# Kernel tuning notes

Hardware: AMD Instinct MI355X
Metric: run time of the kernel (lower is better)

## Reference

```python
import math
import jax, jax.numpy as jnp
import numpy as np

# dims: batch, in-channels, out-channels, features (freq bins), frames, heads, expansion
B, C, CO, F, W, NH, EXP = 1, 8, 8, 512, 256, 8, 4
CC = C + CO          # channels into cross-attn query (cat of h and self_attn)
FC = C + 2 * CO      # channels into FFN (cat of h, self_attn, src_attn)
FH = F * EXP         # FFN hidden features


def mc_linear(x, pw, dw=None):
    # x: [B,Cin,Fin,W]; pw: [Cin,Fout,Fin] per-channel positionwise matmul;
    # dw: [Cout,Cin] channel-mixing matmul ('depthwise' in the repo's naming)
    y = jnp.einsum('bcfw,cgf->bcgw', x, pw)
    if dw is not None:
        y = jnp.einsum('bcgw,oc->bogw', y, dw)
    return y


def frame_conv(x, w, b):
    # Conv2d kernel (1,3), padding (0,1): 1D conv along the frame axis
    y = jax.lax.conv_general_dilated(x, w, (1, 1), ((0, 0), (1, 1)),
                                     dimension_numbers=('NCHW', 'OIHW', 'NCHW'))
    return y + b[None, :, None, None]


def mc_layernorm(x, g, b, eps=1e-5):
    # normalize over the feature axis (2), per (batch, channel, frame)
    mu = x.mean(axis=2, keepdims=True)
    var = jnp.mean(jnp.square(x - mu), axis=2, keepdims=True)
    return (x - mu) * jax.lax.rsqrt(var + eps) * g[None, :, :, None] + b[None, :, :, None]


def mc_attention(xq, xkv, q_pw, q_dw, q_cw, q_cb, k_pw, k_cw, k_cb, v_pw, v_cw, v_cb, o_pw):
    q = frame_conv(mc_linear(xq, q_pw, q_dw), q_cw, q_cb)   # [B,CO,F,Wq]
    k = frame_conv(mc_linear(xkv, k_pw), k_cw, k_cb)        # [B,CO,F,Wk]
    v = frame_conv(mc_linear(xkv, v_pw), v_cw, v_cb)
    dh = F // NH

    def heads(t):  # [B,CO,F,Wt] -> [B,CO,NH,Wt,dh]
        b_, c_, f_, w_ = t.shape
        return t.transpose(0, 1, 3, 2).reshape(b_, c_, w_, NH, dh).transpose(0, 1, 3, 2, 4)

    qh, kh, vh = heads(q), heads(k), heads(v)
    qk = jnp.einsum('bchqd,bchkd->bchqk', qh, kh) / math.sqrt(F)
    a = jnp.einsum('bchqk,bchkd->bchqd', jax.nn.softmax(qk, axis=-1), vh)
    b_, c_, h_, w_, _ = a.shape
    a = a.transpose(0, 1, 3, 2, 4).reshape(b_, c_, w_, F).transpose(0, 1, 3, 2)  # [B,CO,F,Wq]
    return mc_linear(a, o_pw), qk


def setup_inputs() -> dict:
    key = jax.random.key(0)
    ks = jax.random.split(key, 32)
    it = iter(range(32))

    def rn(shape, s=0.02):
        return jax.random.normal(ks[next(it)], shape, jnp.float32) * s

    inp = {
        'x': jax.random.normal(ks[next(it)], (B, C, F, W), jnp.float32),
        'src': jax.random.normal(ks[next(it)], (B, C, F, W), jnp.float32),
        'ln_g': jnp.ones((C, F), jnp.float32),
        'ln_b': jnp.zeros((C, F), jnp.float32),
        # self-attention (C -> CO, C == CO so no channel-mix on projections)
        'sa_q_pw': rn((C, F, F)), 'sa_q_cw': rn((CO, CO, 1, 3), 0.1), 'sa_q_cb': jnp.zeros((CO,), jnp.float32),
        'sa_k_pw': rn((C, F, F)), 'sa_k_cw': rn((CO, CO, 1, 3), 0.1), 'sa_k_cb': jnp.zeros((CO,), jnp.float32),
        'sa_v_pw': rn((C, F, F)), 'sa_v_cw': rn((CO, CO, 1, 3), 0.1), 'sa_v_cb': jnp.zeros((CO,), jnp.float32),
        'sa_o_pw': rn((CO, F, F)),
        # cross-attention (query from CC=C+CO channels -> CO; key/value from src with C channels)
        'ca_q_pw': rn((CC, F, F)), 'ca_q_dw': rn((CO, CC), 0.1),
        'ca_q_cw': rn((CO, CO, 1, 3), 0.1), 'ca_q_cb': jnp.zeros((CO,), jnp.float32),
        'ca_k_pw': rn((C, F, F)), 'ca_k_cw': rn((CO, CO, 1, 3), 0.1), 'ca_k_cb': jnp.zeros((CO,), jnp.float32),
        'ca_v_pw': rn((C, F, F)), 'ca_v_cw': rn((CO, CO, 1, 3), 0.1), 'ca_v_cb': jnp.zeros((CO,), jnp.float32),
        'ca_o_pw': rn((CO, F, F)),
        # FFN
        'ffn1_pw': rn((FC, FH, F)), 'ffn1_dw': rn((FC, FC), 0.1),
        'ffn2_pw': rn((FC, F, FH)), 'ffn2_dw': rn((C, FC), 0.1),
    }
    return inp


def reference(x, src, ln_g, ln_b,
              sa_q_pw, sa_q_cw, sa_q_cb, sa_k_pw, sa_k_cw, sa_k_cb, sa_v_pw, sa_v_cw, sa_v_cb, sa_o_pw,
              ca_q_pw, ca_q_dw, ca_q_cw, ca_q_cb, ca_k_pw, ca_k_cw, ca_k_cb, ca_v_pw, ca_v_cw, ca_v_cb, ca_o_pw,
              ffn1_pw, ffn1_dw, ffn2_pw, ffn2_dw):
    h = mc_layernorm(x, ln_g, ln_b)
    sa, qk1 = mc_attention(h, h, sa_q_pw, None, sa_q_cw, sa_q_cb,
                           sa_k_pw, sa_k_cw, sa_k_cb, sa_v_pw, sa_v_cw, sa_v_cb, sa_o_pw)
    ca, qk2 = mc_attention(jnp.concatenate([h, sa], axis=1), src,
                           ca_q_pw, ca_q_dw, ca_q_cw, ca_q_cb,
                           ca_k_pw, ca_k_cw, ca_k_cb, ca_v_pw, ca_v_cw, ca_v_cb, ca_o_pw)
    z = mc_linear(jnp.concatenate([h, sa, ca], axis=1), ffn1_pw, ffn1_dw)
    z = jax.nn.gelu(z, approximate=False)
    z = mc_linear(z, ffn2_pw, ffn2_dw)
    return (x + z, qk1, qk2)
```

## Files before the change

### kernel.cpp

```cpp
#include <hip/hip_runtime.h>
#include <math.h>

typedef __attribute__((ext_vector_type(4))) float f32x4;
typedef __attribute__((ext_vector_type(8))) short s16x8;
typedef __attribute__((ext_vector_type(4))) short s16x4;

__device__ __forceinline__ unsigned short f2b(float f) {
    union { float f; unsigned u; } v; v.f = f;
    unsigned r = v.u + 0x7fffu + ((v.u >> 16) & 1u);
    return (unsigned short)(r >> 16);
}
__device__ __forceinline__ float b2f(unsigned short u) {
    union { unsigned u; float f; } v; v.u = ((unsigned)u) << 16;
    return v.f;
}

__device__ __forceinline__ void gll16(const void* g, void* l) {
    __builtin_amdgcn_global_load_lds((const __attribute__((address_space(1))) unsigned int*)g,
                                     (__attribute__((address_space(3))) unsigned int*)l,
                                     16, 0, 0);
}

constexpr int kF = 512;
constexpr int kW = 256;
constexpr int kFW = kF * kW;

__global__ __launch_bounds__(256) void prep_kernel(const float* __restrict__ x,
                                                   const float* __restrict__ g,
                                                   const float* __restrict__ b,
                                                   unsigned short* __restrict__ hTb,
                                                   const float* __restrict__ src,
                                                   unsigned short* __restrict__ SRCT) {
    __shared__ float tile[64][65];
    __shared__ float s1[16][16], s2[16][16];
    int bid = blockIdx.x;
    int t = threadIdx.x;
    if (bid < 128) {
        int c = bid >> 4;
        int w0 = (bid & 15) * 16;
        int wi = t & 15, fg = t >> 4;
        const float* xb = x + (size_t)c * kFW + w0 + wi;
        float sum = 0.f, sum2 = 0.f;
        for (int j = 0; j < 32; ++j) {
            float v = xb[(size_t)(fg * 32 + j) * kW];
            sum += v; sum2 += v * v;
        }
        s1[fg][wi] = sum; s2[fg][wi] = sum2;
        __syncthreads();
        float ts = 0.f, tq = 0.f;
        #pragma unroll
        for (int j = 0; j < 16; ++j) { ts += s1[j][wi]; tq += s2[j][wi]; }
        float mu = ts * (1.0f / 512.0f);
        float rstd = rsqrtf(tq * (1.0f / 512.0f) - mu * mu + 1e-5f);
        const float* gc = g + c * kF + fg * 32;
        const float* bc = b + c * kF + fg * 32;
        unsigned short* ob = hTb + (size_t)c * kFW + (size_t)(w0 + wi) * kF + fg * 32;
        for (int j = 0; j < 32; j += 4) {
            float v0 = xb[(size_t)(fg * 32 + j + 0) * kW];
            float v1 = xb[(size_t)(fg * 32 + j + 1) * kW];
            float v2 = xb[(size_t)(fg * 32 + j + 2) * kW];
            float v3 = xb[(size_t)(fg * 32 + j + 3) * kW];
            s16x4 p = { (short)f2b((v0 - mu) * rstd * gc[j + 0] + bc[j + 0]),
                        (short)f2b((v1 - mu) * rstd * gc[j + 1] + bc[j + 1]),
                        (short)f2b((v2 - mu) * rstd * gc[j + 2] + bc[j + 2]),
                        (short)f2b((v3 - mu) * rstd * gc[j + 3] + bc[j + 3]) };
            *(s16x4*)(&ob[j]) = p;
        }
    } else {
        int fid = bid - 128;
        int c = fid >> 5;
        int f0 = ((fid >> 2) & 7) * 64, w0 = (fid & 3) * 64;
        int tw = t & 63, tf4 = t >> 6;
        for (int i = 0; i < 16; ++i) {
            int f = tf4 * 16 + i;
            tile[f][tw] = src[(size_t)c * kFW + (size_t)(f0 + f) * kW + w0 + tw];
        }
        __syncthreads();
        int w = t >> 2, fc = (t & 3) * 16;
        unsigned short* ob = SRCT + (size_t)c * kFW + (size_t)(w0 + w) * kF + f0 + fc;
        for (int j = 0; j < 16; j += 4) {
            s16x4 p = { (short)f2b(tile[fc + j + 0][w]), (short)f2b(tile[fc + j + 1][w]),
                        (short)f2b(tile[fc + j + 2][w]), (short)f2b(tile[fc + j + 3][w]) };
            *(s16x4*)(&ob[j]) = p;
        }
    }
}

struct WSeg { const float* A; const unsigned short* B; void* C; int omode; };
struct WB8 { WSeg s[8]; };

__global__ __launch_bounds__(512) void wgemm512(WB8 wb, int M, int K, int Klocal,
                                                long a_ch, long b_ch, long c_ch, long c_split,
                                                int segshift, int nm, int ksplit) {
    __shared__ unsigned short lds[2][16384];
    int t = threadIdx.x, lane = t & 63, wv = t >> 6;
    int l16 = lane & 15, l4 = lane >> 4;

    int id = blockIdx.x;
    int r = id & 7, j = id >> 3;
    int per = nm * ksplit;
    int y = r + 8 * (j / per);
    int rem = j % per;
    int mt = rem % nm;
    int kz = rem / nm;
    int seg = y >> segshift, c = y & ((1 << segshift) - 1);
    WSeg sg = wb.s[seg];
    int bm = mt * 128;
    int kbase = kz * Klocal;

    const float* A = sg.A + (size_t)c * a_ch + kbase;
    const unsigned short* Bc = sg.B + (size_t)c * b_ch + kbase;
    const float* arow = A + (size_t)(bm + wv * 16 + l16) * K + l4 * 8;

    int rsub = lane >> 3;
    int gsw = ((lane & 7) ^ rsub) * 8;
    const unsigned short* bsrc = Bc + (size_t)(wv * 32 + rsub) * K + gsw;

    f32x4 acc[16];
    #pragma unroll
    for (int i = 0; i < 16; ++i) acc[i] = (f32x4){0.f, 0.f, 0.f, 0.f};

    #pragma unroll
    for (int i = 0; i < 4; ++i)
        gll16(bsrc + (size_t)(i * 8) * K, (char*)lds[0] + ((wv * 32 + i * 8) << 7));

    f32x4 pa0 = __builtin_nontemporal_load((const f32x4*)arow);
    f32x4 pa1 = __builtin_nontemporal_load((const f32x4*)(arow + 4));

    int nc = Klocal >> 6;
    for (int cc = 0; cc < nc; ++cc) {
        __syncthreads();
        if (cc + 1 < nc) {
            int kc = (cc + 1) * 64;
            #pragma unroll
            for (int i = 0; i < 4; ++i)
                gll16(bsrc + (size_t)(i * 8) * K + kc,
                      (char*)lds[(cc + 1) & 1] + ((wv * 32 + i * 8) << 7));
        }
        const unsigned short* buf = lds[cc & 1];
        #pragma unroll
        for (int ks = 0; ks < 2; ++ks) {
            f32x4 c0 = pa0, c1 = pa1;
            int nk = cc * 64 + (ks + 1) * 32;
            if (nk < Klocal) {
                pa0 = __builtin_nontemporal_load((const f32x4*)(arow + nk));
                pa1 = __builtin_nontemporal_load((const f32x4*)(arow + nk + 4));
            }
            s16x8 af = { (short)f2b(c0.x), (short)f2b(c0.y), (short)f2b(c0.z), (short)f2b(c0.w),
                         (short)f2b(c1.x), (short)f2b(c1.y), (short)f2b(c1.z), (short)f2b(c1.w) };
            #pragma unroll
            for (int ni = 0; ni < 16; ++ni) {
                int rr = ni * 16 + l16;
                s16x8 bf = *(const s16x8*)(&buf[rr * 64 + ((ks * 32 + l4 * 8) ^ ((rr & 7) << 3))]);
                acc[ni] = __builtin_amdgcn_mfma_f32_16x16x32_bf16(af, bf, acc[ni], 0, 0, 0);
            }
        }
    }

    int m0 = bm + wv * 16 + l4 * 4;
    if (sg.omode == 2) {
        unsigned short* C = (unsigned short*)sg.C + (size_t)c * c_ch;
        #pragma unroll
        for (int ni = 0; ni < 16; ++ni) {
            int n = ni * 16 + l16;
            s16x4 pk = { (short)f2b(acc[ni][0]), (short)f2b(acc[ni][1]),
                         (short)f2b(acc[ni][2]), (short)f2b(acc[ni][3]) };
            *(s16x4*)(&C[(size_t)n * M + m0]) = pk;
        }
    } else if (sg.omode == 1) {
        unsigned short* C = (unsigned short*)sg.C + (size_t)c * c_ch;
        #pragma unroll
        for (int ni = 0; ni < 16; ++ni) {
            int n = ni * 16 + l16;
            #pragma unroll
            for (int rr = 0; rr < 4; ++rr)
                C[(size_t)(m0 + rr) * 256 + n] = f2b(acc[ni][rr]);
        }
    } else {
        float* C = (float*)sg.C + (size_t)c * c_ch + (size_t)kz * c_split;
        #pragma unroll
        for (int ni = 0; ni < 16; ++ni) {
            int n = ni * 16 + l16;
            #pragma unroll
            for (int rr = 0; rr < 4; ++rr)
                C[(size_t)(m0 + rr) * 256 + n] = acc[ni][rr];
        }
    }
}

__global__ __launch_bounds__(256) void attn_kernel(
    const unsigned short* __restrict__ Qt, const unsigned short* __restrict__ Kt,
    const unsigned short* __restrict__ VN, float* __restrict__ S,
    unsigned short* __restrict__ ATTT, float scale)
{
    __shared__ unsigned short q_lds[4096];
    __shared__ unsigned short kv_lds[16384];
    __shared__ unsigned short p_lds[16384];
    __shared__ float smax[4][64], ssum[4][64], sinv[64];
    int t = threadIdx.x, lane = t & 63, wv = t >> 6;
    int l16 = lane & 15, l4 = lane >> 4;
    int ch = blockIdx.y, c = ch >> 3, h = ch & 7;
    int bm = blockIdx.x * 64;
    const unsigned short* Qb = Qt + (size_t)c * kFW + h * 64;
    const unsigned short* Kb = Kt + (size_t)c * kFW + h * 64;
    const unsigned short* Vb = VN + (size_t)c * kFW + (size_t)(h * 64) * 256;
    float* Sb = S + (size_t)ch * 65536;
    unsigned short* Ab = ATTT + (size_t)c * kFW + h * 64;

    s16x8 qr[2], kr[8], vr[8];
    #pragma unroll
    for (int i = 0; i < 2; ++i) {
        int idx = i * 256 + t; int rr = idx >> 3, ck = idx & 7;
        qr[i] = *(const s16x8*)(Qb + (size_t)(bm + rr) * 512 + ck * 8);
    }
    #pragma unroll
    for (int i = 0; i < 8; ++i) {
        int idx = i * 256 + t; int rr = idx >> 3, ck = idx & 7;
        kr[i] = *(const s16x8*)(Kb + (size_t)rr * 512 + ck * 8);
    }
    #pragma unroll
    for (int i = 0; i < 8; ++i) {
        int idx = i * 256 + t; int d = idx >> 5, cs = idx & 31;
        vr[i] = *(const s16x8*)(Vb + (size_t)d * 256 + cs * 8);
    }
    #pragma unroll
    for (int i = 0; i < 2; ++i) {
        int idx = i * 256 + t; int rr = idx >> 3, ck = idx & 7;
        *(s16x8*)(&q_lds[rr * 64 + ((ck * 8) ^ ((rr & 7) << 3))]) = qr[i];
    }
    #pragma unroll
    for (int i = 0; i < 8; ++i) {
        int idx = i * 256 + t; int rr = idx >> 3, ck = idx & 7;
        *(s16x8*)(&kv_lds[rr * 64 + ((ck * 8) ^ ((rr & 7) << 3))]) = kr[i];
    }
    __syncthreads();

    f32x4 acc[4][4];
    #pragma unroll
    for (int i = 0; i < 4; ++i)
        #pragma unroll
        for (int jj = 0; jj < 4; ++jj) acc[i][jj] = (f32x4){0.f, 0.f, 0.f, 0.f};
    #pragma unroll
    for (int ks = 0; ks < 2; ++ks) {
        s16x8 af[4], bfr[4];
        #pragma unroll
        for (int mi = 0; mi < 4; ++mi) {
            int rq = mi * 16 + l16;
            af[mi] = *(const s16x8*)(&q_lds[rq * 64 + ((ks * 32 + l4 * 8) ^ ((rq & 7) << 3))]);
        }
        #pragma unroll
        for (int ni = 0; ni < 4; ++ni) {
            int rk = wv * 64 + ni * 16 + l16;
            bfr[ni] = *(const s16x8*)(&kv_lds[rk * 64 + ((ks * 32 + l4 * 8) ^ ((rk & 7) << 3))]);
        }
        #pragma unroll
        for (int mi = 0; mi < 4; ++mi)
            #pragma unroll
            for (int ni = 0; ni < 4; ++ni)
                acc[mi][ni] = __builtin_amdgcn_mfma_f32_16x16x32_bf16(af[mi], bfr[ni], acc[mi][ni], 0, 0, 0);
    }

    #pragma unroll
    for (int mi = 0; mi < 4; ++mi)
        #pragma unroll
        for (int ni = 0; ni < 4; ++ni) {
            acc[mi][ni] *= scale;
            int col = wv * 64 + ni * 16 + l16;
            int row0 = bm + mi * 16 + l4 * 4;
            #pragma unroll
            for (int rr = 0; rr < 4; ++rr)
                Sb[(size_t)(row0 + rr) * 256 + col] = acc[mi][ni][rr];
        }

    float rmax[4][4];
    #pragma unroll
    for (int mi = 0; mi < 4; ++mi)
        #pragma unroll
        for (int rr = 0; rr < 4; ++rr)
            rmax[mi][rr] = fmaxf(fmaxf(acc[mi][0][rr], acc[mi][1][rr]), fmaxf(acc[mi][2][rr], acc[mi][3][rr]));
    #pragma unroll
    for (int d = 1; d < 16; d <<= 1)
        #pragma unroll
        for (int mi = 0; mi < 4; ++mi)
            #pragma unroll
            for (int rr = 0; rr < 4; ++rr)
                rmax[mi][rr] = fmaxf(rmax[mi][rr], __shfl_xor(rmax[mi][rr], d));
    if (l16 == 0)
        #pragma unroll
        for (int mi = 0; mi < 4; ++mi)
            #pragma unroll
            for (int rr = 0; rr < 4; ++rr)
                smax[wv][mi * 16 + l4 * 4 + rr] = rmax[mi][rr];
    __syncthreads();
    float rsum[4][4];
    #pragma unroll
    for (int mi = 0; mi < 4; ++mi)
        #pragma unroll
        for (int rr = 0; rr < 4; ++rr) {
            int row = mi * 16 + l4 * 4 + rr;
            float rM = fmaxf(fmaxf(smax[0][row], smax[1][row]), fmaxf(smax[2][row], smax[3][row]));
            rsum[mi][rr] = 0.f;
            #pragma unroll
            for (int ni = 0; ni < 4; ++ni) {
                float e = __expf(acc[mi][ni][rr] - rM);
                acc[mi][ni][rr] = e;
                rsum[mi][rr] += e;
            }
        }
    #pragma unroll
    for (int d = 1; d < 16; d <<= 1)
        #pragma unroll
        for (int mi = 0; mi < 4; ++mi)
            #pragma unroll
            for (int rr = 0; rr < 4; ++rr)
                rsum[mi][rr] += __shfl_xor(rsum[mi][rr], d);
    if (l16 == 0)
        #pragma unroll
        for (int mi = 0; mi < 4; ++mi)
            #pragma unroll
            for (int rr = 0; rr < 4; ++rr)
                ssum[wv][mi * 16 + l4 * 4 + rr] = rsum[mi][rr];
    __syncthreads();

    #pragma unroll
    for (int i = 0; i < 8; ++i) {
        int idx = i * 256 + t; int d = idx >> 5, cs = idx & 31;
        *(s16x8*)(&kv_lds[d * 256 + ((cs * 8) ^ ((d & 7) << 3))]) = vr[i];
    }
    #pragma unroll
    for (int mi = 0; mi < 4; ++mi)
        #pragma unroll
        for (int ni = 0; ni < 4; ++ni) {
            int col = wv * 64 + ni * 16 + l16;
            int cb = col & ~7, cl = col & 7;
            #pragma unroll
            for (int rr = 0; rr < 4; ++rr) {
                int row = mi * 16 + l4 * 4 + rr;
                p_lds[row * 256 + (cb ^ ((row & 7) << 3)) + cl] = f2b(acc[mi][ni][rr]);
            }
        }
    if (t < 64) sinv[t] = 1.f / (ssum[0][t] + ssum[1][t] + ssum[2][t] + ssum[3][t]);
    __syncthreads();

    f32x4 po[4];
    #pragma unroll
    for (int ni = 0; ni < 4; ++ni) po[ni] = (f32x4){0.f, 0.f, 0.f, 0.f};
    int qrow = wv * 16 + l16;
    #pragma unroll
    for (int ks = 0; ks < 8; ++ks) {
        s16x8 paf = *(const s16x8*)(&p_lds[qrow * 256 + ((ks * 32 + l4 * 8) ^ ((qrow & 7) << 3))]);
        #pragma unroll
        for (int ni = 0; ni < 4; ++ni) {
            int rd = ni * 16 + l16;
            s16x8 bf = *(const s16x8*)(&kv_lds[rd * 256 + ((ks * 32 + l4 * 8) ^ ((rd & 7) << 3))]);
            po[ni] = __builtin_amdgcn_mfma_f32_16x16x32_bf16(paf, bf, po[ni], 0, 0, 0);
        }
    }
    #pragma unroll
    for (int ni = 0; ni < 4; ++ni) {
        int d = ni * 16 + l16;
        #pragma unroll
        for (int rr = 0; rr < 4; ++rr) {
            int row = wv * 16 + l4 * 4 + rr;
            Ab[(size_t)(bm + row) * 512 + d] = f2b(po[ni][rr] * sinv[row]);
        }
    }
}

struct ConvArgs {
    const unsigned short* in[5];
    unsigned short* out[5];
    const float* cw[5];
    const float* cb[5];
    int mode[5];
};

__global__ __launch_bounds__(256) void conv5_kernel(ConvArgs a) {
    int g = blockIdx.y;
    __shared__ float scw[192]; __shared__ float scb[8];
    int t = threadIdx.x;
    if (t < 192) scw[t] = a.cw[g][t];
    if (t >= 192 && t < 200) scb[t - 192] = a.cb[g][t - 192];
    __syncthreads();
    const unsigned short* in = a.in[g];
    unsigned short* out = a.out[g];
    int gi = blockIdx.x * 256 + t;
    int mode = a.mode[g];
    int w = mode ? (gi & 255) : (gi >> 9);
    int str = mode ? 1 : 512;
    float acc[8];
    #pragma unroll
    for (int o = 0; o < 8; ++o) acc[o] = scb[o];
    bool hm = w > 0, hp = w < 255;
    #pragma unroll
    for (int i = 0; i < 8; ++i) {
        size_t base = (size_t)i * kFW + gi;
        float xm = hm ? b2f(in[base - str]) : 0.f;
        float x0 = b2f(in[base]);
        float xp = hp ? b2f(in[base + str]) : 0.f;
        #pragma unroll
        for (int o = 0; o < 8; ++o) {
            const float* wp = &scw[(o * 8 + i) * 3];
            acc[o] += wp[0] * xm + wp[1] * x0 + wp[2] * xp;
        }
    }
    #pragma unroll
    for (int o = 0; o < 8; ++o) out[(size_t)o * kFW + gi] = f2b(acc[o]);
}

__global__ __launch_bounds__(256) void mixconv_kernel(const unsigned short* __restrict__ in,
                                                      const float* __restrict__ dw,
                                                      const float* __restrict__ cw,
                                                      const float* __restrict__ cb,
                                                      unsigned short* __restrict__ out) {
    __shared__ float sdw[128], scw[192], scb[8];
    int t = threadIdx.x;
    if (t < 128) sdw[t] = dw[t];
    if (t >= 128 && t < 136) scb[t - 128] = cb[t - 128];
    if (t < 192) scw[t] = cw[t];
    __syncthreads();
    int gi = blockIdx.x * 256 + t;
    int w = gi >> 9;
    bool hm = w > 0, hp = w < 255;
    float xc[16], xm[16], xp[16];
    #pragma unroll
    for (int cc = 0; cc < 16; ++cc) {
        size_t base = (size_t)cc * kFW + gi;
        xc[cc] = b2f(in[base]);
        xm[cc] = hm ? b2f(in[base - 512]) : 0.f;
        xp[cc] = hp ? b2f(in[base + 512]) : 0.f;
    }
    float mm[8], m0[8], mp[8];
    #pragma unroll
    for (int o = 0; o < 8; ++o) {
        float am = 0.f, a0 = 0.f, ap = 0.f;
        #pragma unroll
        for (int cc = 0; cc < 16; ++cc) {
            float wv = sdw[o * 16 + cc];
            am += wv * xm[cc]; a0 += wv * xc[cc]; ap += wv * xp[cc];
        }
        mm[o] = am; m0[o] = a0; mp[o] = ap;
    }
    #pragma unroll
    for (int o = 0; o < 8; ++o) {
        float acc = scb[o];
        #pragma unroll
        for (int i = 0; i < 8; ++i) {
            const float* wp = &scw[(o * 8 + i) * 3];
            acc += wp[0] * mm[i] + wp[1] * m0[i] + wp[2] * mp[i];
        }
        out[(size_t)o * kFW + gi] = f2b(acc);
    }
}

__global__ __launch_bounds__(256) void gelu24_kernel(unsigned short* __restrict__ z,
                                                     const float* __restrict__ dw) {
    __shared__ float sdw[576];
    int t = threadIdx.x;
    for (int i = t; i < 576; i += 256) sdw[i] = dw[i];
    __syncthreads();
    size_t gi = (size_t)blockIdx.x * 256 + t;
    const size_t CH = (size_t)256 * 2048;
    float xv[24];
    #pragma unroll
    for (int cc = 0; cc < 24; ++cc) xv[cc] = b2f(z[cc * CH + gi]);
    #pragma unroll
    for (int o = 0; o < 24; ++o) {
        float s = 0.f;
        #pragma unroll
        for (int cc = 0; cc < 24; ++cc) s += sdw[o * 24 + cc] * xv[cc];
        s = 0.5f * s * (1.0f + erff(s * 0.7071067811865475f));
        z[o * CH + gi] = f2b(s);
    }
}

__global__ __launch_bounds__(256) void final_mix_add2(const float* __restrict__ x,
                                                      const float* __restrict__ z2,
                                                      const float* __restrict__ dw,
                                                      float* __restrict__ out) {
    __shared__ float sdw[192];
    int t = threadIdx.x;
    if (t < 192) sdw[t] = dw[t];
    __syncthreads();
    int gi = blockIdx.x * 256 + t;
    const size_t PSZ = (size_t)24 * kFW;
    float xv[24];
    #pragma unroll
    for (int cc = 0; cc < 24; ++cc) {
        size_t o = (size_t)cc * kFW + gi;
        xv[cc] = z2[o] + z2[PSZ + o];
    }
    #pragma unroll
    for (int o = 0; o < 8; ++o) {
        float s = 0.f;
        #pragma unroll
        for (int cc = 0; cc < 24; ++cc) s += sdw[o * 24 + cc] * xv[cc];
        out[(size_t)o * kFW + gi] = x[(size_t)o * kFW + gi] + s;
    }
}

extern "C" void kernel_launch(void* const* d_in, const int* in_sizes, int n_in,
                              void* d_out, int out_size, void* d_ws, size_t ws_size,
                              hipStream_t stream) {
    const float* x       = (const float*)d_in[0];
    const float* src     = (const float*)d_in[1];
    const float* ln_g    = (const float*)d_in[2];
    const float* ln_b    = (const float*)d_in[3];
    const float* sa_q_pw = (const float*)d_in[4];
    const float* sa_q_cw = (const float*)d_in[5];
    const float* sa_q_cb = (const float*)d_in[6];
    const float* sa_k_pw = (const float*)d_in[7];
    const float* sa_k_cw = (const float*)d_in[8];
    const float* sa_k_cb = (const float*)d_in[9];
    const float* sa_v_pw = (const float*)d_in[10];
    const float* sa_v_cw = (const float*)d_in[11];
    const float* sa_v_cb = (const float*)d_in[12];
    const float* sa_o_pw = (const float*)d_in[13];
    const float* ca_q_pw = (const float*)d_in[14];
    const float* ca_q_dw = (const float*)d_in[15];
    const float* ca_q_cw = (const float*)d_in[16];
    const float* ca_q_cb = (const float*)d_in[17];
    const float* ca_k_pw = (const float*)d_in[18];
    const float* ca_k_cw = (const float*)d_in[19];
    const float* ca_k_cb = (const float*)d_in[20];
    const float* ca_v_pw = (const float*)d_in[21];
    const float* ca_v_cw = (const float*)d_in[22];
    const float* ca_v_cb = (const float*)d_in[23];
    const float* ca_o_pw = (const float*)d_in[24];
    const float* ffn1_pw = (const float*)d_in[25];
    const float* ffn1_dw = (const float*)d_in[26];
    const float* ffn2_pw = (const float*)d_in[27];
    const float* ffn2_dw = (const float*)d_in[28];

    float* out  = (float*)d_out;
    float* qk1o = out + 1048576;
    float* qk2o = out + 1048576 + 4194304;

    unsigned char* ws = (unsigned char*)d_ws;
    unsigned short* CAT24  = (unsigned short*)(ws + 0);
    unsigned short* hTb    = CAT24;
    unsigned short* saTb   = CAT24 + 8 * (size_t)kFW;
    unsigned short* caTb   = CAT24 + 16 * (size_t)kFW;
    unsigned short* SRCT   = (unsigned short*)(ws + 6291456);
    unsigned short* preQ   = (unsigned short*)(ws + 8388608);
    unsigned short* preK   = (unsigned short*)(ws + 10485760);
    unsigned short* preVsa = (unsigned short*)(ws + 12582912);
    unsigned short* preKca = (unsigned short*)(ws + 14680064);
    unsigned short* preVca = (unsigned short*)(ws + 16777216);
    unsigned short* QT     = (unsigned short*)(ws + 18874368);
    unsigned short* KT     = (unsigned short*)(ws + 20971520);
    unsigned short* VNsa   = (unsigned short*)(ws + 23068672);
    unsigned short* KTca   = (unsigned short*)(ws + 25165824);
    unsigned short* VNca   = (unsigned short*)(ws + 27262976);
    unsigned short* PRE16  = (unsigned short*)(ws + 29360128);
    unsigned short* QTca   = (unsigned short*)(ws + 33554432);
    unsigned short* ATTT   = (unsigned short*)(ws + 35651584);
    unsigned short* Z0T    = (unsigned short*)(ws + 8388608);
    float*          Z2P    = (float*)(ws + 37748736);

    const float qscale = 0.044194173824159216f;
    dim3 blk(256);
    dim3 blk512(512);

    prep_kernel<<<384, blk, 0, stream>>>(x, ln_g, ln_b, hTb, src, SRCT);

    WB8 p6;
    p6.s[0] = { sa_q_pw, hTb,  preQ,   2 };
    p6.s[1] = { sa_k_pw, hTb,  preK,   2 };
    p6.s[2] = { sa_v_pw, hTb,  preVsa, 1 };
    p6.s[3] = { ca_k_pw, SRCT, preKca, 2 };
    p6.s[4] = { ca_v_pw, SRCT, preVca, 1 };
    p6.s[5] = { ca_q_pw, hTb,  PRE16,  2 };
    p6.s[6] = p6.s[0]; p6.s[7] = p6.s[0];
    wgemm512<<<dim3(192), blk512, 0, stream>>>(p6, 512, 512, 512, 262144, kFW, kFW, 0, 3, 4, 1);

    ConvArgs c5;
    c5.in[0] = preQ;   c5.out[0] = QT;   c5.cw[0] = sa_q_cw; c5.cb[0] = sa_q_cb; c5.mode[0] = 0;
    c5.in[1] = preK;   c5.out[1] = KT;   c5.cw[1] = sa_k_cw; c5.cb[1] = sa_k_cb; c5.mode[1] = 0;
    c5.in[2] = preVsa; c5.out[2] = VNsa; c5.cw[2] = sa_v_cw; c5.cb[2] = sa_v_cb; c5.mode[2] = 1;
    c5.in[3] = preKca; c5.out[3] = KTca; c5.cw[3] = ca_k_cw; c5.cb[3] = ca_k_cb; c5.mode[3] = 0;
    c5.in[4] = preVca; c5.out[4] = VNca; c5.cw[4] = ca_v_cw; c5.cb[4] = ca_v_cb; c5.mode[4] = 1;
    conv5_kernel<<<dim3(512, 5), blk, 0, stream>>>(c5);

    attn_kernel<<<dim3(4, 64), blk, 0, stream>>>(QT, KT, VNsa, qk1o, ATTT, qscale);
    WB8 so;
    so.s[0] = { sa_o_pw, ATTT, saTb, 2 };
    for (int i = 1; i < 8; ++i) so.s[i] = so.s[0];
    wgemm512<<<dim3(32), blk512, 0, stream>>>(so, 512, 512, 512, 262144, kFW, kFW, 0, 8, 4, 1);

    WB8 cq2;
    cq2.s[0] = { ca_q_pw + 8 * 262144, saTb, PRE16 + 8 * (size_t)kFW, 2 };
    for (int i = 1; i < 8; ++i) cq2.s[i] = cq2.s[0];
    wgemm512<<<dim3(32), blk512, 0, stream>>>(cq2, 512, 512, 512, 262144, kFW, kFW, 0, 8, 4, 1);
    mixconv_kernel<<<512, blk, 0, stream>>>(PRE16, ca_q_dw, ca_q_cw, ca_q_cb, QTca);

    attn_kernel<<<dim3(4, 64), blk, 0, stream>>>(QTca, KTca, VNca, qk2o, ATTT, qscale);
    WB8 co;
    co.s[0] = { ca_o_pw, ATTT, caTb, 2 };
    for (int i = 1; i < 8; ++i) co.s[i] = co.s[0];
    wgemm512<<<dim3(32), blk512, 0, stream>>>(co, 512, 512, 512, 262144, kFW, kFW, 0, 8, 4, 1);

    WB8 f1;
    f1.s[0] = { ffn1_pw, CAT24, Z0T, 2 };
    for (int i = 1; i < 8; ++i) f1.s[i] = f1.s[0];
    wgemm512<<<dim3(384), blk512, 0, stream>>>(f1, 2048, 512, 512, 1048576, kFW, 524288, 0, 8, 16, 1);
    gelu24_kernel<<<2048, blk, 0, stream>>>(Z0T, ffn1_dw);
    WB8 f2;
    f2.s[0] = { ffn2_pw, Z0T, Z2P, 0 };
    for (int i = 1; i < 8; ++i) f2.s[i] = f2.s[0];
    wgemm512<<<dim3(192), blk512, 0, stream>>>(f2, 512, 2048, 1024, 1048576, 524288, kFW, 3145728, 8, 4, 2);
    final_mix_add2<<<512, blk, 0, stream>>>(x, Z2P, ffn2_dw, out);
}
```

Before: 285.9 us.

## Add smaller-tile 256-thread GEMM variant to spread small projections over more blocks

Introduces a templated wgemmT kernel with 64-row M tiles and configurable N tile width (256 or 128), using 256 threads and a single LDS buffer. It replaces the 512-thread wgemm512 for the six-segment QKV projection and the three small 8-channel GEMMs (self-attn output, cross-attn query second half, cross-attn output). The small GEMMs launch 128 blocks instead of 32, and the QKV GEMM launches 384 instead of 192, aiming to fill more CUs on the MI355X. The trade-off is less data reuse per block and no double-buffering of the B tile.

```diff
diff --git a/kernel.cpp b/kernel.cpp
--- a/kernel.cpp
+++ b/kernel.cpp
@@ -88,6 +88,106 @@
 
 struct WSeg { const float* A; const unsigned short* B; void* C; int omode; };
 struct WB8 { WSeg s[8]; };
+
+template<int BN>
+__global__ __launch_bounds__(256) void wgemmT(WB8 wb, int M, int K, int Klocal,
+                                              long a_ch, long b_ch, long c_ch, long c_split,
+                                              int segshift, int nm, int ntiles, int ksplit) {
+    constexpr int NF = BN / 16;
+    constexpr int RPW = BN / 4;
+    constexpr int GP = BN / 32;
+    __shared__ unsigned short lds[BN * 64];
+
+    int t = threadIdx.x, lane = t & 63, wv = t >> 6;
+    int l16 = lane & 15, l4 = lane >> 4;
+
+    int id = blockIdx.x;
+    int r = id & 7, j = id >> 3;
+    int per = nm * ntiles * ksplit;
+    int y = r + 8 * (j / per);
+    int rem = j % per;
+    int mt = rem % nm;
+    int rem2 = rem / nm;
+    int ntile = rem2 % ntiles;
+    int kz = rem2 / ntiles;
+    int seg = y >> segshift, c = y & ((1 << segshift) - 1);
+    WSeg sg = wb.s[seg];
+    int bm = mt * 64;
+    int bn = ntile * BN;
+    int kbase = kz * Klocal;
+
+    const float* A = sg.A + (size_t)c * a_ch + kbase;
+    const unsigned short* Bc = sg.B + (size_t)c * b_ch + kbase;
+    const float* arow = A + (size_t)(bm + wv * 16 + l16) * K + l4 * 8;
+
+    int rsub = lane >> 3;
+    int gsw = ((lane & 7) ^ rsub) * 8;
+    const unsigned short* bsrc = Bc + (size_t)(bn + wv * RPW + rsub) * K + gsw;
+
+    f32x4 acc[NF];
+    #pragma unroll
+    for (int i = 0; i < NF; ++i) acc[i] = (f32x4){0.f, 0.f, 0.f, 0.f};
+
+    f32x4 pa0 = __builtin_nontemporal_load((const f32x4*)arow);
+    f32x4 pa1 = __builtin_nontemporal_load((const f32x4*)(arow + 4));
+
+    for (int kc = 0; kc < Klocal; kc += 64) {
+        if (kc) __syncthreads();
+        #pragma unroll
+        for (int i = 0; i < GP; ++i) {
+            int r0 = wv * RPW + i * 8;
+            gll16(bsrc + (size_t)(i * 8) * K + kc, (char*)lds + (r0 << 7));
+        }
+        __syncthreads();
+        #pragma unroll
+        for (int ks = 0; ks < 2; ++ks) {
+            f32x4 c0 = pa0, c1 = pa1;
+            int nk = kc + (ks + 1) * 32;
+            if (nk < Klocal) {
+                pa0 = __builtin_nontemporal_load((const f32x4*)(arow + nk));
+                pa1 = __builtin_nontemporal_load((const f32x4*)(arow + nk + 4));
+            }
+            s16x8 af = { (short)f2b(c0.x), (short)f2b(c0.y), (short)f2b(c0.z), (short)f2b(c0.w),
+                         (short)f2b(c1.x), (short)f2b(c1.y), (short)f2b(c1.z), (short)f2b(c1.w) };
+            #pragma unroll
+            for (int ni = 0; ni < NF; ++ni) {
+                int rr = ni * 16 + l16;
+                s16x8 bf = *(const s16x8*)(&lds[rr * 64 + ((ks * 32 + l4 * 8) ^ ((rr & 7) << 3))]);
+                acc[ni] = __builtin_amdgcn_mfma_f32_16x16x32_bf16(af, bf, acc[ni], 0, 0, 0);
+            }
+        }
+    }
+
+    int m0 = bm + wv * 16 + l4 * 4;
+    if (sg.omode == 2) {
+        unsigned short* C = (unsigned short*)sg.C + (size_t)c * c_ch;
+        #pragma unroll
+        for (int ni = 0; ni < NF; ++ni) {
+            int n = bn + ni * 16 + l16;
+            s16x4 pk = { (short)f2b(acc[ni][0]), (short)f2b(acc[ni][1]),
+                         (short)f2b(acc[ni][2]), (short)f2b(acc[ni][3]) };
+            *(s16x4*)(&C[(size_t)n * M + m0]) = pk;
+        }
+    } else if (sg.omode == 1) {
+        unsigned short* C = (unsigned short*)sg.C + (size_t)c * c_ch;
+        #pragma unroll
+        for (int ni = 0; ni < NF; ++ni) {
+            int n = bn + ni * 16 + l16;
+            #pragma unroll
+            for (int rr = 0; rr < 4; ++rr)
+                C[(size_t)(m0 + rr) * 256 + n] = f2b(acc[ni][rr]);
+        }
+    } else {
+        float* C = (float*)sg.C + (size_t)c * c_ch + (size_t)kz * c_split;
+        #pragma unroll
+        for (int ni = 0; ni < NF; ++ni) {
+            int n = bn + ni * 16 + l16;
+            #pragma unroll
+            for (int rr = 0; rr < 4; ++rr)
+                C[(size_t)(m0 + rr) * 256 + n] = acc[ni][rr];
+        }
+    }
+}
 
 __global__ __launch_bounds__(512) void wgemm512(WB8 wb, int M, int K, int Klocal,
                                                 long a_ch, long b_ch, long c_ch, long c_split,
@@ -572,7 +672,7 @@
     p6.s[4] = { ca_v_pw, SRCT, preVca, 1 };
     p6.s[5] = { ca_q_pw, hTb,  PRE16,  2 };
     p6.s[6] = p6.s[0]; p6.s[7] = p6.s[0];
-    wgemm512<<<dim3(192), blk512, 0, stream>>>(p6, 512, 512, 512, 262144, kFW, kFW, 0, 3, 4, 1);
+    wgemmT<256><<<dim3(384), blk, 0, stream>>>(p6, 512, 512, 512, 262144, kFW, kFW, 0, 3, 8, 1, 1);
 
     ConvArgs c5;
     c5.in[0] = preQ;   c5.out[0] = QT;   c5.cw[0] = sa_q_cw; c5.cb[0] = sa_q_cb; c5.mode[0] = 0;
@@ -586,19 +686,19 @@
     WB8 so;
     so.s[0] = { sa_o_pw, ATTT, saTb, 2 };
     for (int i = 1; i < 8; ++i) so.s[i] = so.s[0];
-    wgemm512<<<dim3(32), blk512, 0, stream>>>(so, 512, 512, 512, 262144, kFW, kFW, 0, 8, 4, 1);
+    wgemmT<128><<<dim3(128), blk, 0, stream>>>(so, 512, 512, 512, 262144, kFW, kFW, 0, 8, 8, 2, 1);
 
     WB8 cq2;
     cq2.s[0] = { ca_q_pw + 8 * 262144, saTb, PRE16 + 8 * (size_t)kFW, 2 };
     for (int i = 1; i < 8; ++i) cq2.s[i] = cq2.s[0];
-    wgemm512<<<dim3(32), blk512, 0, stream>>>(cq2, 512, 512, 512, 262144, kFW, kFW, 0, 8, 4, 1);
+    wgemmT<128><<<dim3(128), blk, 0, stream>>>(cq2, 512, 512, 512, 262144, kFW, kFW, 0, 8, 8, 2, 1);
     mixconv_kernel<<<512, blk, 0, stream>>>(PRE16, ca_q_dw, ca_q_cw, ca_q_cb, QTca);
 
     attn_kernel<<<dim3(4, 64), blk, 0, stream>>>(QTca, KTca, VNca, qk2o, ATTT, qscale);
     WB8 co;
     co.s[0] = { ca_o_pw, ATTT, caTb, 2 };
     for (int i = 1; i < 8; ++i) co.s[i] = co.s[0];
-    wgemm512<<<dim3(32), blk512, 0, stream>>>(co, 512, 512, 512, 262144, kFW, kFW, 0, 8, 4, 1);
+    wgemmT<128><<<dim3(128), blk, 0, stream>>>(co, 512, 512, 512, 262144, kFW, kFW, 0, 8, 8, 2, 1);
 
     WB8 f1;
     f1.s[0] = { ffn1_pw, CAT24, Z0T, 2 };
```

Result: faster. 268.5 us (-6.1%).

## Template GEMM over N-tile and M-tile sizes, split N, and pipeline A loads

Applied to the files above, without the earlier changes.

The bf16 MFMA GEMM becomes a template over BN/BM tiles with a new N-tile grid dimension. Every launch now splits the 256-wide N into two 128-wide tiles, and the small output-projection GEMMs use 64-row M tiles with 256 threads. Together these raise the block count so more CUs are busy. The A-operand prefetch now loads a whole 64-wide K chunk one iteration ahead, and __syncthreads is replaced by an explicit vmcnt wait plus s_barrier to overlap loads with MFMA. The trade-off is that each B tile is loaded once per N-tile, so A is reloaded twice, and the hand-written waitcnt depends on the exact order in which loads are issued.

```diff
diff --git a/kernel.cpp b/kernel.cpp
--- a/kernel.cpp
+++ b/kernel.cpp
@@ -89,23 +89,32 @@
 struct WSeg { const float* A; const unsigned short* B; void* C; int omode; };
 struct WB8 { WSeg s[8]; };
 
-__global__ __launch_bounds__(512) void wgemm512(WB8 wb, int M, int K, int Klocal,
-                                                long a_ch, long b_ch, long c_ch, long c_split,
-                                                int segshift, int nm, int ksplit) {
-    __shared__ unsigned short lds[2][16384];
+template<int BN, int BM>
+__global__ __launch_bounds__(BM * 4) void wgemmDB(WB8 wb, int M, int K, int Klocal,
+                                                  long a_ch, long b_ch, long c_ch, long c_split,
+                                                  int segshift, int nm, int ntiles, int ksplit) {
+    constexpr int WAVES = BM / 16;
+    constexpr int NF = BN / 16;
+    constexpr int RPW = BN / WAVES;
+    constexpr int GP = RPW / 8;
+    __shared__ unsigned short lds[2][BN * 64];
+
     int t = threadIdx.x, lane = t & 63, wv = t >> 6;
     int l16 = lane & 15, l4 = lane >> 4;
 
     int id = blockIdx.x;
     int r = id & 7, j = id >> 3;
-    int per = nm * ksplit;
+    int per = nm * ntiles * ksplit;
     int y = r + 8 * (j / per);
     int rem = j % per;
     int mt = rem % nm;
-    int kz = rem / nm;
+    int rem2 = rem / nm;
+    int ntile = rem2 % ntiles;
+    int kz = rem2 / ntiles;
     int seg = y >> segshift, c = y & ((1 << segshift) - 1);
     WSeg sg = wb.s[seg];
-    int bm = mt * 128;
+    int bm = mt * BM;
+    int bn = ntile * BN;
     int kbase = kz * Klocal;
 
     const float* A = sg.A + (size_t)c * a_ch + kbase;
@@ -114,55 +123,68 @@
 
     int rsub = lane >> 3;
     int gsw = ((lane & 7) ^ rsub) * 8;
-    const unsigned short* bsrc = Bc + (size_t)(wv * 32 + rsub) * K + gsw;
-
-    f32x4 acc[16];
-    #pragma unroll
-    for (int i = 0; i < 16; ++i) acc[i] = (f32x4){0.f, 0.f, 0.f, 0.f};
-
-    #pragma unroll
-    for (int i = 0; i < 4; ++i)
-        gll16(bsrc + (size_t)(i * 8) * K, (char*)lds[0] + ((wv * 32 + i * 8) << 7));
-
-    f32x4 pa0 = __builtin_nontemporal_load((const f32x4*)arow);
-    f32x4 pa1 = __builtin_nontemporal_load((const f32x4*)(arow + 4));
+    const unsigned short* bsrc = Bc + (size_t)(bn + wv * RPW + rsub) * K + gsw;
+
+    f32x4 acc[NF];
+    #pragma unroll
+    for (int i = 0; i < NF; ++i) acc[i] = (f32x4){0.f, 0.f, 0.f, 0.f};
+
+    #pragma unroll
+    for (int i = 0; i < GP; ++i)
+        gll16(bsrc + (size_t)(i * 8) * K, (char*)lds[0] + ((wv * RPW + i * 8) << 7));
+    __builtin_amdgcn_sched_barrier(0);
+    f32x4 ca0 = __builtin_nontemporal_load((const f32x4*)(arow));
+    f32x4 ca1 = __builtin_nontemporal_load((const f32x4*)(arow + 4));
+    f32x4 ca2 = __builtin_nontemporal_load((const f32x4*)(arow + 32));
+    f32x4 ca3 = __builtin_nontemporal_load((const f32x4*)(arow + 36));
+    f32x4 na0 = ca0, na1 = ca1, na2 = ca2, na3 = ca3;
 
     int nc = Klocal >> 6;
     for (int cc = 0; cc < nc; ++cc) {
-        __syncthreads();
+        __builtin_amdgcn_sched_barrier(0);
+        asm volatile("s_waitcnt vmcnt(4)" ::: "memory");
+        __builtin_amdgcn_s_barrier();
+        __builtin_amdgcn_sched_barrier(0);
         if (cc + 1 < nc) {
             int kc = (cc + 1) * 64;
             #pragma unroll
-            for (int i = 0; i < 4; ++i)
+            for (int i = 0; i < GP; ++i)
                 gll16(bsrc + (size_t)(i * 8) * K + kc,
-                      (char*)lds[(cc + 1) & 1] + ((wv * 32 + i * 8) << 7));
+                      (char*)lds[(cc + 1) & 1] + ((wv * RPW + i * 8) << 7));
+            __builtin_amdgcn_sched_barrier(0);
+            na0 = __builtin_nontemporal_load((const f32x4*)(arow + kc));
+            na1 = __builtin_nontemporal_load((const f32x4*)(arow + kc + 4));
+            na2 = __builtin_nontemporal_load((const f32x4*)(arow + kc + 32));
+            na3 = __builtin_nontemporal_load((const f32x4*)(arow + kc + 36));
         }
         const unsigned short* buf = lds[cc & 1];
-        #pragma unroll
-        for (int ks = 0; ks < 2; ++ks) {
-            f32x4 c0 = pa0, c1 = pa1;
-            int nk = cc * 64 + (ks + 1) * 32;
-            if (nk < Klocal) {
-                pa0 = __builtin_nontemporal_load((const f32x4*)(arow + nk));
-                pa1 = __builtin_nontemporal_load((const f32x4*)(arow + nk + 4));
-            }
-            s16x8 af = { (short)f2b(c0.x), (short)f2b(c0.y), (short)f2b(c0.z), (short)f2b(c0.w),
-                         (short)f2b(c1.x), (short)f2b(c1.y), (short)f2b(c1.z), (short)f2b(c1.w) };
-            #pragma unroll
-            for (int ni = 0; ni < 16; ++ni) {
+        {
+            s16x8 af = { (short)f2b(ca0.x), (short)f2b(ca0.y), (short)f2b(ca0.z), (short)f2b(ca0.w),
+                         (short)f2b(ca1.x), (short)f2b(ca1.y), (short)f2b(ca1.z), (short)f2b(ca1.w) };
+            #pragma unroll
+            for (int ni = 0; ni < NF; ++ni) {
                 int rr = ni * 16 + l16;
-                s16x8 bf = *(const s16x8*)(&buf[rr * 64 + ((ks * 32 + l4 * 8) ^ ((rr & 7) << 3))]);
+                s16x8 bf = *(const s16x8*)(&buf[rr * 64 + ((l4 * 8) ^ ((rr & 7) << 3))]);
                 acc[ni] = __builtin_amdgcn_mfma_f32_16x16x32_bf16(af, bf, acc[ni], 0, 0, 0);
             }
-        }
+            s16x8 af1 = { (short)f2b(ca2.x), (short)f2b(ca2.y), (short)f2b(ca2.z), (short)f2b(ca2.w),
+                          (short)f2b(ca3.x), (short)f2b(ca3.y), (short)f2b(ca3.z), (short)f2b(ca3.w) };
+            #pragma unroll
+            for (int ni = 0; ni < NF; ++ni) {
+                int rr = ni * 16 + l16;
+                s16x8 bf = *(const s16x8*)(&buf[rr * 64 + ((32 + l4 * 8) ^ ((rr & 7) << 3))]);
+                acc[ni] = __builtin_amdgcn_mfma_f32_16x16x32_bf16(af1, bf, acc[ni], 0, 0, 0);
+            }
+        }
+        ca0 = na0; ca1 = na1; ca2 = na2; ca3 = na3;
     }
 
     int m0 = bm + wv * 16 + l4 * 4;
     if (sg.omode == 2) {
         unsigned short* C = (unsigned short*)sg.C + (size_t)c * c_ch;
         #pragma unroll
-        for (int ni = 0; ni < 16; ++ni) {
-            int n = ni * 16 + l16;
+        for (int ni = 0; ni < NF; ++ni) {
+            int n = bn + ni * 16 + l16;
             s16x4 pk = { (short)f2b(acc[ni][0]), (short)f2b(acc[ni][1]),
                          (short)f2b(acc[ni][2]), (short)f2b(acc[ni][3]) };
             *(s16x4*)(&C[(size_t)n * M + m0]) = pk;
@@ -170,8 +192,8 @@
     } else if (sg.omode == 1) {
         unsigned short* C = (unsigned short*)sg.C + (size_t)c * c_ch;
         #pragma unroll
-        for (int ni = 0; ni < 16; ++ni) {
-            int n = ni * 16 + l16;
+        for (int ni = 0; ni < NF; ++ni) {
+            int n = bn + ni * 16 + l16;
             #pragma unroll
             for (int rr = 0; rr < 4; ++rr)
                 C[(size_t)(m0 + rr) * 256 + n] = f2b(acc[ni][rr]);
@@ -179,8 +201,8 @@
     } else {
         float* C = (float*)sg.C + (size_t)c * c_ch + (size_t)kz * c_split;
         #pragma unroll
-        for (int ni = 0; ni < 16; ++ni) {
-            int n = ni * 16 + l16;
+        for (int ni = 0; ni < NF; ++ni) {
+            int n = bn + ni * 16 + l16;
             #pragma unroll
             for (int rr = 0; rr < 4; ++rr)
                 C[(size_t)(m0 + rr) * 256 + n] = acc[ni][rr];
@@ -572,7 +594,8 @@
     p6.s[4] = { ca_v_pw, SRCT, preVca, 1 };
     p6.s[5] = { ca_q_pw, hTb,  PRE16,  2 };
     p6.s[6] = p6.s[0]; p6.s[7] = p6.s[0];
-    wgemm512<<<dim3(192), blk512, 0, stream>>>(p6, 512, 512, 512, 262144, kFW, kFW, 0, 3, 4, 1);
+    wgemmDB<128, 128><<<dim3(384), blk512, 0, stream>>>(p6, 512, 512, 512,
+        262144, kFW, kFW, 0, 3, 4, 2, 1);
 
     ConvArgs c5;
     c5.in[0] = preQ;   c5.out[0] = QT;   c5.cw[0] = sa_q_cw; c5.cb[0] = sa_q_cb; c5.mode[0] = 0;
@@ -586,28 +609,33 @@
     WB8 so;
     so.s[0] = { sa_o_pw, ATTT, saTb, 2 };
     for (int i = 1; i < 8; ++i) so.s[i] = so.s[0];
-    wgemm512<<<dim3(32), blk512, 0, stream>>>(so, 512, 512, 512, 262144, kFW, kFW, 0, 8, 4, 1);
+    wgemmDB<128, 64><<<dim3(128), blk, 0, stream>>>(so, 512, 512, 512,
+        262144, kFW, kFW, 0, 8, 8, 2, 1);
 
     WB8 cq2;
     cq2.s[0] = { ca_q_pw + 8 * 262144, saTb, PRE16 + 8 * (size_t)kFW, 2 };
     for (int i = 1; i < 8; ++i) cq2.s[i] = cq2.s[0];
-    wgemm512<<<dim3(32), blk512, 0, stream>>>(cq2, 512, 512, 512, 262144, kFW, kFW, 0, 8, 4, 1);
+    wgemmDB<128, 64><<<dim3(128), blk, 0, stream>>>(cq2, 512, 512, 512,
+        262144, kFW, kFW, 0, 8, 8, 2, 1);
     mixconv_kernel<<<512, blk, 0, stream>>>(PRE16, ca_q_dw, ca_q_cw, ca_q_cb, QTca);
 
     attn_kernel<<<dim3(4, 64), blk, 0, stream>>>(QTca, KTca, VNca, qk2o, ATTT, qscale);
     WB8 co;
     co.s[0] = { ca_o_pw, ATTT, caTb, 2 };
     for (int i = 1; i < 8; ++i) co.s[i] = co.s[0];
-    wgemm512<<<dim3(32), blk512, 0, stream>>>(co, 512, 512, 512, 262144, kFW, kFW, 0, 8, 4, 1);
+    wgemmDB<128, 64><<<dim3(128), blk, 0, stream>>>(co, 512, 512, 512,
+        262144, kFW, kFW, 0, 8, 8, 2, 1);
 
     WB8 f1;
     f1.s[0] = { ffn1_pw, CAT24, Z0T, 2 };
     for (int i = 1; i < 8; ++i) f1.s[i] = f1.s[0];
-    wgemm512<<<dim3(384), blk512, 0, stream>>>(f1, 2048, 512, 512, 1048576, kFW, 524288, 0, 8, 16, 1);
+    wgemmDB<128, 128><<<dim3(768), blk512, 0, stream>>>(f1, 2048, 512, 512,
+        1048576, kFW, 524288, 0, 8, 16, 2, 1);
     gelu24_kernel<<<2048, blk, 0, stream>>>(Z0T, ffn1_dw);
     WB8 f2;
     f2.s[0] = { ffn2_pw, Z0T, Z2P, 0 };
     for (int i = 1; i < 8; ++i) f2.s[i] = f2.s[0];
-    wgemm512<<<dim3(192), blk512, 0, stream>>>(f2, 512, 2048, 1024, 1048576, 524288, kFW, 3145728, 8, 4, 2);
+    wgemmDB<128, 128><<<dim3(384), blk512, 0, stream>>>(f2, 512, 2048, 1024,
+        1048576, 524288, kFW, 3145728, 8, 4, 2, 2);
     final_mix_add2<<<512, blk, 0, stream>>>(x, Z2P, ffn2_dw, out);
 }
```

After: 285.7 us. No clear change (-0.1%).
